# Performance work log

Hardware: AMD Instinct MI355X
Metric: run time of the kernel (lower is better)

The kernel has to match this reference:

```python
import jax, jax.numpy as jnp
import numpy as np

C = 32          # d_model / channels
D_STATE = 32
D_CONV = 4
EXPAND = 2
D_INNER = EXPAND * C          # 64
DT_RANK = (C + 15) // 16      # ceil(32/16) = 2
EPS = 1e-5


def _conv2d(x, w, b):
    # x: (B,C,H,W), w: (O,I,3,3), stride 1, padding 1 (torch Conv2d)
    y = jax.lax.conv_general_dilated(
        x, w, window_strides=(1, 1), padding=[(1, 1), (1, 1)],
        dimension_numbers=("NCHW", "OIHW", "NCHW"))
    return y + b[None, :, None, None]


def _silu(x):
    return x * jax.nn.sigmoid(x)


def _mamba(xs, in_proj_w, conv1d_w, conv1d_b, x_proj_w, dt_proj_w, dt_proj_b,
           A_log, Dp, out_proj_w):
    # xs: (B, L, C)
    xz = xs @ in_proj_w.T                       # (B, L, 2*D_INNER)
    xm, z = jnp.split(xz, 2, axis=-1)           # each (B, L, D_INNER)

    # causal depthwise conv1d along L (torch: padding=d_conv-1 then [..., :L])
    xc = xm.transpose(0, 2, 1)                  # (B, D_INNER, L)
    xc = jax.lax.conv_general_dilated(
        xc, conv1d_w, window_strides=(1,), padding=[(D_CONV - 1, 0)],
        dimension_numbers=("NCH", "OIH", "NCH"),
        feature_group_count=D_INNER)
    xm = _silu((xc + conv1d_b[None, :, None]).transpose(0, 2, 1))  # (B,L,D_INNER)

    x_dbl = xm @ x_proj_w.T                     # (B, L, DT_RANK + 2*D_STATE)
    dt = x_dbl[..., :DT_RANK]
    Bm = x_dbl[..., DT_RANK:DT_RANK + D_STATE]  # (B, L, N)
    Cm = x_dbl[..., DT_RANK + D_STATE:]         # (B, L, N)

    delta = jax.nn.softplus(dt @ dt_proj_w.T + dt_proj_b)  # (B, L, D_INNER)
    A = -jnp.exp(A_log)                                     # (D_INNER, N)

    deltaA = jnp.exp(delta[..., None] * A)                           # (B,L,D,N)
    deltaBx = delta[..., None] * Bm[:, :, None, :] * xm[..., None]   # (B,L,D,N)

    def combine(c1, c2):
        a1, b1 = c1
        a2, b2 = c2
        return a1 * a2, a2 * b1 + b2

    # parallel linear recurrence h_t = deltaA_t * h_{t-1} + deltaBx_t
    _, hstate = jax.lax.associative_scan(combine, (deltaA, deltaBx), axis=1)

    y = jnp.einsum("bldn,bln->bld", hstate, Cm) + xm * Dp
    y = y * _silu(z)
    return y @ out_proj_w.T                     # (B, L, C)


def setup_inputs() -> dict:
    key = jax.random.key(0)
    ks = jax.random.split(key, 16)
    s = 0.02
    inp = {
        "x": jax.random.normal(ks[0], (4, C, 64, 64), dtype=jnp.float32),
        "conv1_w": jax.random.normal(ks[1], (2 * C, C, 3, 3), jnp.float32) * s,
        "conv1_b": jnp.zeros((2 * C,), jnp.float32),
        "conv2_w": jax.random.normal(ks[2], (C, 2 * C, 3, 3), jnp.float32) * s,
        "conv2_b": jnp.zeros((C,), jnp.float32),
        "ln_g": jnp.ones((C,), jnp.float32),
        "ln_b": jnp.zeros((C,), jnp.float32),
        "in_proj_w": jax.random.normal(ks[3], (2 * D_INNER, C), jnp.float32) * s,
        "conv1d_w": jax.random.normal(ks[4], (D_INNER, 1, D_CONV), jnp.float32) * 0.1,
        "conv1d_b": jnp.zeros((D_INNER,), jnp.float32),
        "x_proj_w": jax.random.normal(ks[5], (DT_RANK + 2 * D_STATE, D_INNER), jnp.float32) * s,
        "dt_proj_w": jax.random.normal(ks[6], (D_INNER, DT_RANK), jnp.float32) * 0.1,
        "dt_proj_b": jax.random.normal(ks[7], (D_INNER,), jnp.float32) * 0.1 - 4.0,
        "A_log": jnp.log(jnp.tile(jnp.arange(1, D_STATE + 1, dtype=jnp.float32), (D_INNER, 1))),
        "Dp": jnp.ones((D_INNER,), jnp.float32),
        "out_proj_w": jax.random.normal(ks[8], (C, D_INNER), jnp.float32) * s,
        "smooth_w": jax.random.normal(ks[9], (C, C, 3, 3), jnp.float32) * s,
        "smooth_b": jnp.zeros((C,), jnp.float32),
    }
    return inp


def reference(x, conv1_w, conv1_b, conv2_w, conv2_b, ln_g, ln_b,
              in_proj_w, conv1d_w, conv1d_b, x_proj_w, dt_proj_w, dt_proj_b,
              A_log, Dp, out_proj_w, smooth_w, smooth_b):
    b, c, h, w = x.shape
    # convb residual
    t = jax.nn.relu(_conv2d(x, conv1_w, conv1_b))
    x = _conv2d(t, conv2_w, conv2_b) + x
    # reshape (b,c,h,w) -> (b, h*w, c) row-major (faithful to torch .reshape)
    xs = x.reshape(b, -1, c)
    # LayerNorm over last dim
    mu = jnp.mean(xs, axis=-1, keepdims=True)
    var = jnp.mean(jnp.square(xs - mu), axis=-1, keepdims=True)
    xs = (xs - mu) * jax.lax.rsqrt(var + EPS) * ln_g + ln_b
    # Mamba block
    y = _mamba(xs, in_proj_w, conv1d_w, conv1d_b, x_proj_w, dt_proj_w,
               dt_proj_b, A_log, Dp, out_proj_w)
    y = y.transpose(0, 2, 1).reshape(b, c, h, w)
    return _conv2d(y, smooth_w, smooth_b)
```

## Files before the change

### kernel.cpp

```cpp
#include <hip/hip_runtime.h>
#include <math.h>

#define SEQL 4096
#define L2E 1.44269504088896340736f

#if defined(__has_builtin)
#if __has_builtin(__builtin_amdgcn_exp2f)
#define FAST_EXP2(x) __builtin_amdgcn_exp2f(x)
#endif
#endif
#ifndef FAST_EXP2
#define FAST_EXP2(x) exp2f(x)
#endif

__device__ __forceinline__ float sigmoid_f(float x){ return 1.0f/(1.0f+expf(-x)); }

template<int CI, int CO, int COW, bool RELU, bool RES>
__global__ __launch_bounds__(512, 2) void conv3x3_k(const float* __restrict__ in,
    const float* __restrict__ wgt, const float* __restrict__ bias,
    const float* __restrict__ res, float* __restrict__ out)
{
  __shared__ __align__(16) float tin[CI][3][72];
  const int tid  = threadIdx.x;
  const int lane = tid & 63;
  const int ty   = tid >> 6;
  const int tyu  = __builtin_amdgcn_readfirstlane(ty);
  const int h0   = blockIdx.x;
  const int b    = blockIdx.y;
  const int co0  = tyu*COW;

  constexpr int NF4 = CI*48;
  #pragma unroll
  for (int k=0; k<NF4/512; ++k){
    int i   = tid + (k<<9);
    int ci  = i / 48;
    int rem = i - ci*48;
    int row = rem >> 4;
    int w4  = (rem & 15) << 2;
    int h   = h0 - 1 + row;
    float4 v = make_float4(0.f,0.f,0.f,0.f);
    if (h>=0 && h<64)
      v = *(const float4*)(in + ((size_t)(b*CI+ci)*64 + h)*64 + w4);
    *(float4*)&tin[ci][row][4+w4] = v;
    if (w4 == 0)  tin[ci][row][3]  = 0.0f;
    if (w4 == 60) tin[ci][row][68] = 0.0f;
  }
  __syncthreads();

  float acc[COW];
  #pragma unroll
  for (int u=0;u<COW;++u) acc[u] = 0.0f;

  #pragma unroll 2
  for (int ci=0; ci<CI; ++ci){
    float rv[3][3];
    #pragma unroll
    for (int r=0;r<3;++r)
      #pragma unroll
      for (int c=0;c<3;++c)
        rv[r][c] = tin[ci][r][3+lane+c];
    #pragma unroll
    for (int u=0;u<COW;++u){
      const float* wp = wgt + ((size_t)(co0+u)*CI + ci)*9;
      #pragma unroll
      for (int r=0;r<3;++r){
        acc[u] = fmaf(rv[r][0], wp[3*r+0], acc[u]);
        acc[u] = fmaf(rv[r][1], wp[3*r+1], acc[u]);
        acc[u] = fmaf(rv[r][2], wp[3*r+2], acc[u]);
      }
    }
  }

  #pragma unroll
  for (int u=0;u<COW;++u){
    float s = acc[u] + bias[co0+u];
    size_t ob = ((size_t)(b*CO+co0+u)*64 + h0)*64 + lane;
    if constexpr (RES)  s += res[ob];
    if constexpr (RELU) s = fmaxf(s, 0.0f);
    out[ob] = s;
  }
}

__global__ __launch_bounds__(1024, 4) void mamba_in_k(const float* __restrict__ x2,
    const float* __restrict__ g, const float* __restrict__ be,
    const float* __restrict__ Wip, const float* __restrict__ cw,
    const float* __restrict__ cb, const float* __restrict__ Wxp,
    const float* __restrict__ Wdt, const float* __restrict__ bdt,
    const float* __restrict__ A_log,
    float* __restrict__ xm2, float* __restrict__ szb, float* __restrict__ dlt,
    float* __restrict__ Bm, float* __restrict__ Cm,
    float* __restrict__ cA, float* __restrict__ cH)
{
  __shared__ __align__(16) float xn[68][37];
  __shared__ __align__(16) float xm[64][68];
  __shared__ __align__(16) float xtT[64][68];
  __shared__ __align__(16) float xd[64][67];
  float (*xbT)[68] = reinterpret_cast<float(*)[68]>(&xn[0][0]);
  const int tid = threadIdx.x, lane = tid & 63, ty = tid >> 6;
  const int tyu = __builtin_amdgcn_readfirstlane(ty);
  const int bi = blockIdx.x >> 6;
  const int l0 = (blockIdx.x & 63) << 6;

  {
    const int row = tid >> 3, sub = tid & 7;
    if (row < 67){
      const int tok = l0 - 3 + row;
      const int c0 = sub << 2;
      if (tok >= 0){
        float4 f = *(const float4*)(x2 + (size_t)bi*131072 + (size_t)tok*32 + c0);
        float s = (f.x+f.y)+(f.z+f.w);
        s += __shfl_xor(s,1); s += __shfl_xor(s,2); s += __shfl_xor(s,4);
        const float mu = s * 0.03125f;
        float dx=f.x-mu, dy=f.y-mu, dz=f.z-mu, dw=f.w-mu;
        float q = (dx*dx+dy*dy)+(dz*dz+dw*dw);
        q += __shfl_xor(q,1); q += __shfl_xor(q,2); q += __shfl_xor(q,4);
        const float rstd = 1.0f/sqrtf(q*0.03125f + 1e-5f);
        float4 gv = *(const float4*)(g  + c0);
        float4 bv = *(const float4*)(be + c0);
        xn[row][c0+0] = dx*rstd*gv.x + bv.x;
        xn[row][c0+1] = dy*rstd*gv.y + bv.y;
        xn[row][c0+2] = dz*rstd*gv.z + bv.z;
        xn[row][c0+3] = dw*rstd*gv.w + bv.w;
      } else {
        xn[row][c0+0]=0.0f; xn[row][c0+1]=0.0f;
        xn[row][c0+2]=0.0f; xn[row][c0+3]=0.0f;
      }
    }
  }
  __syncthreads();

  if (ty < 8){
    const int d0 = tyu*8;
    float xvA[32];
    #pragma unroll
    for (int c=0;c<32;++c) xvA[c] = xn[lane][c];
    #pragma unroll
    for (int jj=0;jj<8;++jj){
      const float4* wr = (const float4*)(Wip + (d0+jj)*32);
      float a = 0.0f;
      #pragma unroll
      for (int c4=0;c4<8;++c4){
        float4 w = wr[c4];
        a = fmaf(xvA[c4*4+0], w.x, a);
        a = fmaf(xvA[c4*4+1], w.y, a);
        a = fmaf(xvA[c4*4+2], w.z, a);
        a = fmaf(xvA[c4*4+3], w.w, a);
      }
      xm[d0+jj][lane] = a;
    }
    if (lane < 3){
      float xvB[32];
      #pragma unroll
      for (int c=0;c<32;++c) xvB[c] = xn[64+lane][c];
      #pragma unroll
      for (int jj=0;jj<8;++jj){
        const float4* wr = (const float4*)(Wip + (d0+jj)*32);
        float a = 0.0f;
        #pragma unroll
        for (int c4=0;c4<8;++c4){
          float4 w = wr[c4];
          a = fmaf(xvB[c4*4+0], w.x, a);
          a = fmaf(xvB[c4*4+1], w.y, a);
          a = fmaf(xvB[c4*4+2], w.z, a);
          a = fmaf(xvB[c4*4+3], w.w, a);
        }
        xm[d0+jj][64+lane] = a;
      }
    }
  } else {
    const int d0z = (tyu-8)*8;
    float xvC[32];
    #pragma unroll
    for (int c=0;c<32;++c) xvC[c] = xn[lane+3][c];
    #pragma unroll
    for (int jj=0;jj<8;++jj){
      const float4* wr = (const float4*)(Wip + (64+d0z+jj)*32);
      float a = 0.0f;
      #pragma unroll
      for (int c4=0;c4<8;++c4){
        float4 w = wr[c4];
        a = fmaf(xvC[c4*4+0], w.x, a);
        a = fmaf(xvC[c4*4+1], w.y, a);
        a = fmaf(xvC[c4*4+2], w.z, a);
        a = fmaf(xvC[c4*4+3], w.w, a);
      }
      szb[((size_t)(bi*64+d0z+jj))*SEQL + l0 + lane] = a * sigmoid_f(a);
    }
  }
  __syncthreads();

  #pragma unroll
  for (int jj=0;jj<4;++jj){
    int d = tyu*4 + jj;
    float4 w = *(const float4*)(cw + d*4);
    float a = xm[d][lane]*w.x + xm[d][lane+1]*w.y
            + xm[d][lane+2]*w.z + xm[d][lane+3]*w.w + cb[d];
    float s = a * sigmoid_f(a);
    xtT[d][lane] = s;
    xm2[((size_t)(bi*64+d))*SEQL + l0 + lane] = s;
  }
  __syncthreads();

  {
    float xv[64];
    #pragma unroll
    for (int c=0;c<64;++c) xv[c] = xtT[c][lane];
    for (int j=tyu; j<66; j+=16){
      const float4* wr = (const float4*)(Wxp + j*64);
      float a = 0.0f;
      #pragma unroll
      for (int c4=0;c4<16;++c4){
        float4 w = wr[c4];
        a = fmaf(xv[c4*4+0], w.x, a);
        a = fmaf(xv[c4*4+1], w.y, a);
        a = fmaf(xv[c4*4+2], w.z, a);
        a = fmaf(xv[c4*4+3], w.w, a);
      }
      xd[lane][j] = a;
    }
  }
  __syncthreads();

  {
    float dt0 = xd[lane][0], dt1 = xd[lane][1];
    #pragma unroll
    for (int k=0;k<4;++k){
      int d2 = tyu*4 + k;
      float2 wd = *(const float2*)(Wdt + d2*2);
      float v = dt0*wd.x + dt1*wd.y + bdt[d2];
      float sp = fmaxf(v,0.0f) + log1pf(expf(-fabsf(v)));
      dlt[((size_t)(bi*64+d2))*SEQL + l0 + lane] = sp;
      xm[d2][lane] = sp;
    }
    const int which = tyu >> 3, gq = tyu & 7;
    float* dst = which ? Cm : Bm;
    size_t base = ((size_t)bi*SEQL + l0 + lane)*32 + gq*4;
    const int s2 = 2 + which*32;
    float4 f0;
    f0.x = xd[lane][s2+gq+ 0]; f0.y = xd[lane][s2+gq+ 8];
    f0.z = xd[lane][s2+gq+16]; f0.w = xd[lane][s2+gq+24];
    *(float4*)(dst + base) = f0;
    if (!which){
      xbT[gq     ][lane] = f0.x;
      xbT[gq +  8][lane] = f0.y;
      xbT[gq + 16][lane] = f0.z;
      xbT[gq + 24][lane] = f0.w;
    }
  }
  __syncthreads();

  {
    const int d  = tid >> 4;
    const int gg = tid & 15;
    const int chunk = blockIdx.x & 63;
    const int bd = bi*64 + d;
    float Av0 = -expf(A_log[d*32 + gg     ]) * L2E;
    float Av1 = -expf(A_log[d*32 + gg + 16]) * L2E;
    float h0=0.0f, h1=0.0f, aP0=1.0f, aP1=1.0f;
    #pragma unroll 2
    for (int t0=0;t0<64;t0+=4){
      float4 dl4 = *(const float4*)&xm [d    ][t0];
      float4 xs4 = *(const float4*)&xtT[d    ][t0];
      float4 b04 = *(const float4*)&xbT[gg   ][t0];
      float4 b14 = *(const float4*)&xbT[gg+16][t0];
      #pragma unroll
      for (int k=0;k<4;++k){
        float dlv = (k==0)? dl4.x : (k==1)? dl4.y : (k==2)? dl4.z : dl4.w;
        float xsv = (k==0)? xs4.x : (k==1)? xs4.y : (k==2)? xs4.z : xs4.w;
        float bv0 = (k==0)? b04.x : (k==1)? b04.y : (k==2)? b04.z : b04.w;
        float bv1 = (k==0)? b14.x : (k==1)? b14.y : (k==2)? b14.z : b14.w;
        float m  = dlv * xsv;
        float a0 = FAST_EXP2(dlv*Av0);
        float a1 = FAST_EXP2(dlv*Av1);
        h0 = fmaf(a0, h0, m*bv0);  aP0 *= a0;
        h1 = fmaf(a1, h1, m*bv1);  aP1 *= a1;
      }
    }
    size_t base = ((size_t)bd*64 + chunk)*32;
    cA[base + gg] = aP0; cA[base + gg + 16] = aP1;
    cH[base + gg] = h0;  cH[base + gg + 16] = h1;
  }
}

__global__ __launch_bounds__(256) void scan_p2(const float* __restrict__ dlt,
    const float* __restrict__ xssm, const float* __restrict__ Bm,
    const float* __restrict__ Cm, const float* __restrict__ A_log,
    const float* __restrict__ Dp, const float* __restrict__ sz,
    const float* __restrict__ cA, const float* __restrict__ cHs,
    float* __restrict__ yt)
{
  __shared__ float pre[32][34];
  const int tid = threadIdx.x;
  const int grp = blockIdx.x & 1;
  const int bd  = blockIdx.x >> 1;
  const int b = bd >> 6, d = bd & 63;
  const int c0 = grp << 5;

  if (tid < 32){
    const float* pa = cA  + (size_t)bd*2048 + tid;
    const float* ph = cHs + (size_t)bd*2048 + tid;
    float hrun = 0.0f;
    if (grp){
      #pragma unroll 4
      for (int c=0;c<32;++c)
        hrun = fmaf(pa[c*32], hrun, ph[c*32]);
    }
    #pragma unroll 4
    for (int k=0;k<32;++k){
      pre[tid][k] = hrun;
      hrun = fmaf(pa[(c0+k)*32], hrun, ph[(c0+k)*32]);
    }
  }
  __syncthreads();

  const int lc = tid >> 3, gg = tid & 7;
  const int chunk = c0 + lc;
  const int l0 = chunk << 6;
  const float Dv = Dp[d];
  float Av2[4], h[4];
  #pragma unroll
  for (int j=0;j<4;++j){
    Av2[j] = -expf(A_log[d*32 + gg + 8*j]) * L2E;
    h[j] = pre[gg + 8*j][lc];
  }
  const float* del = dlt  + (size_t)bd*SEQL + l0;
  const float* xp  = xssm + (size_t)bd*SEQL + l0;
  const float* szp = sz   + (size_t)bd*SEQL + l0;
  const float* Bp  = Bm + ((size_t)b*SEQL + l0)*32 + gg*4;
  const float* Cp  = Cm + ((size_t)b*SEQL + l0)*32 + gg*4;
  float* yp = yt + (size_t)bd*SEQL + l0;

  for (int i0=0;i0<64;i0+=16){
    float4 y4[4];
    #pragma unroll
    for (int s=0;s<4;++s){
      const int ib = i0 + s*4;
      float4 d4 = *(const float4*)(del+ib);
      float4 x4 = *(const float4*)(xp +ib);
      float4 s4 = *(const float4*)(szp+ib);
      #pragma unroll
      for (int t=0;t<4;++t){
        float dl = (t==0)? d4.x : (t==1)? d4.y : (t==2)? d4.z : d4.w;
        float xl = (t==0)? x4.x : (t==1)? x4.y : (t==2)? x4.z : x4.w;
        float sl = (t==0)? s4.x : (t==1)? s4.y : (t==2)? s4.z : s4.w;
        float4 bv = *(const float4*)(Bp + (ib+t)*32);
        float4 cv = *(const float4*)(Cp + (ib+t)*32);
        float a0 = FAST_EXP2(dl*Av2[0]); h[0] = fmaf(a0, h[0], dl*bv.x*xl);
        float a1 = FAST_EXP2(dl*Av2[1]); h[1] = fmaf(a1, h[1], dl*bv.y*xl);
        float a2 = FAST_EXP2(dl*Av2[2]); h[2] = fmaf(a2, h[2], dl*bv.z*xl);
        float a3 = FAST_EXP2(dl*Av2[3]); h[3] = fmaf(a3, h[3], dl*bv.w*xl);
        float v = fmaf(h[3], cv.w, fmaf(h[2], cv.z, fmaf(h[1], cv.y, h[0]*cv.x)));
        v += __shfl_xor(v,1); v += __shfl_xor(v,2); v += __shfl_xor(v,4);
        float yv = fmaf(xl, Dv, v) * sl;
        if      (t==0) y4[s].x = yv;
        else if (t==1) y4[s].y = yv;
        else if (t==2) y4[s].z = yv;
        else           y4[s].w = yv;
      }
    }
    if (gg < 4){
      float4 w = (gg==0) ? y4[0] : (gg==1) ? y4[1] : (gg==2) ? y4[2] : y4[3];
      *(float4*)(yp + i0 + gg*4) = w;
    }
  }
}

__global__ __launch_bounds__(512) void outproj_k(const float* __restrict__ yt,
    const float* __restrict__ Wout, float* __restrict__ ym)
{
  __shared__ float ys[64][67];
  const int tid = threadIdx.x, lane = tid & 63, ty = tid >> 6;
  const int tyu = __builtin_amdgcn_readfirstlane(ty);
  const int bi = blockIdx.x >> 6;
  const int l0 = (blockIdx.x & 63) << 6;
  for (int r=ty; r<64; r+=8)
    ys[lane][r] = yt[((size_t)(bi*64+r))*SEQL + l0 + lane];
  __syncthreads();
  float yv[64];
  #pragma unroll
  for (int c=0;c<64;++c) yv[c] = ys[lane][c];
  #pragma unroll
  for (int jj=0;jj<4;++jj){
    int j = tyu*4 + jj;
    const float4* wr = (const float4*)(Wout + j*64);
    float acc = 0.0f;
    #pragma unroll
    for (int c4=0;c4<16;++c4){
      float4 w = wr[c4];
      acc = fmaf(yv[c4*4+0], w.x, acc);
      acc = fmaf(yv[c4*4+1], w.y, acc);
      acc = fmaf(yv[c4*4+2], w.z, acc);
      acc = fmaf(yv[c4*4+3], w.w, acc);
    }
    ym[((size_t)(bi*32+j))*SEQL + l0 + lane] = acc;
  }
}

extern "C" void kernel_launch(void* const* d_in, const int* in_sizes, int n_in,
                              void* d_out, int out_size, void* d_ws, size_t ws_size,
                              hipStream_t stream) {
  const float* x        = (const float*)d_in[0];
  const float* conv1_w  = (const float*)d_in[1];
  const float* conv1_b  = (const float*)d_in[2];
  const float* conv2_w  = (const float*)d_in[3];
  const float* conv2_b  = (const float*)d_in[4];
  const float* ln_g     = (const float*)d_in[5];
  const float* ln_b     = (const float*)d_in[6];
  const float* in_proj_w= (const float*)d_in[7];
  const float* conv1d_w = (const float*)d_in[8];
  const float* conv1d_b = (const float*)d_in[9];
  const float* x_proj_w = (const float*)d_in[10];
  const float* dt_proj_w= (const float*)d_in[11];
  const float* dt_proj_b= (const float*)d_in[12];
  const float* A_log    = (const float*)d_in[13];
  const float* Dp       = (const float*)d_in[14];
  const float* out_proj_w=(const float*)d_in[15];
  const float* smooth_w = (const float*)d_in[16];
  const float* smooth_b = (const float*)d_in[17];
  float* out = (float*)d_out;

  float* ws = (float*)d_ws;
  float* t      = ws;
  float* x2     = t      + 1048576;
  float* xm2    = x2     + 524288;
  float* szb    = xm2    + 1048576;
  float* dlt    = szb    + 1048576;
  float* Bmat   = dlt    + 1048576;
  float* Cmat   = Bmat   + 524288;
  float* yt     = Cmat   + 524288;
  float* ym     = yt     + 1048576;
  float* cA     = t;
  float* cH     = t + 524288;

  conv3x3_k<32,64,8,true ,false><<<dim3(64,4), 512, 0, stream>>>(x,  conv1_w, conv1_b, nullptr, t);
  conv3x3_k<64,32,4,false,true ><<<dim3(64,4), 512, 0, stream>>>(t,  conv2_w, conv2_b, x,       x2);
  mamba_in_k  <<<256, 1024, 0, stream>>>(x2, ln_g, ln_b, in_proj_w, conv1d_w, conv1d_b,
                                         x_proj_w, dt_proj_w, dt_proj_b, A_log,
                                         xm2, szb, dlt, Bmat, Cmat, cA, cH);
  scan_p2     <<<512, 256, 0, stream>>>(dlt, xm2, Bmat, Cmat, A_log, Dp, szb, cA, cH, yt);
  outproj_k   <<<256, 512, 0, stream>>>(yt, out_proj_w, ym);
  conv3x3_k<32,32,4,false,false><<<dim3(64,4), 512, 0, stream>>>(ym, smooth_w, smooth_b, nullptr, out);
}
```

Baseline: 219.4 us.

## Replace LDS-staged conv3x3 with direct global loads and wave shuffles

```diff
diff --git a/kernel.cpp b/kernel.cpp
--- a/kernel.cpp
+++ b/kernel.cpp
@@ -15,64 +15,48 @@
 
 __device__ __forceinline__ float sigmoid_f(float x){ return 1.0f/(1.0f+expf(-x)); }
 
-template<int CI, int CO, int COW, bool RELU, bool RES>
-__global__ __launch_bounds__(512, 2) void conv3x3_k(const float* __restrict__ in,
+template<int CI, int CO, int COG, bool RELU, bool RES>
+__global__ __launch_bounds__(256) void conv3x3_k(const float* __restrict__ in,
     const float* __restrict__ wgt, const float* __restrict__ bias,
     const float* __restrict__ res, float* __restrict__ out)
 {
-  __shared__ __align__(16) float tin[CI][3][72];
   const int tid  = threadIdx.x;
   const int lane = tid & 63;
   const int ty   = tid >> 6;
   const int tyu  = __builtin_amdgcn_readfirstlane(ty);
   const int h0   = blockIdx.x;
-  const int b    = blockIdx.y;
-  const int co0  = tyu*COW;
-
-  constexpr int NF4 = CI*48;
-  #pragma unroll
-  for (int k=0; k<NF4/512; ++k){
-    int i   = tid + (k<<9);
-    int ci  = i / 48;
-    int rem = i - ci*48;
-    int row = rem >> 4;
-    int w4  = (rem & 15) << 2;
-    int h   = h0 - 1 + row;
-    float4 v = make_float4(0.f,0.f,0.f,0.f);
-    if (h>=0 && h<64)
-      v = *(const float4*)(in + ((size_t)(b*CI+ci)*64 + h)*64 + w4);
-    *(float4*)&tin[ci][row][4+w4] = v;
-    if (w4 == 0)  tin[ci][row][3]  = 0.0f;
-    if (w4 == 60) tin[ci][row][68] = 0.0f;
-  }
-  __syncthreads();
-
-  float acc[COW];
-  #pragma unroll
-  for (int u=0;u<COW;++u) acc[u] = 0.0f;
+  const int co0  = (blockIdx.y*4 + tyu)*COG;
+  const int b    = blockIdx.z;
+
+  float acc[COG];
+  #pragma unroll
+  for (int u=0;u<COG;++u) acc[u] = 0.0f;
+
+  const float* inb = in + (size_t)b*CI*4096;
 
   #pragma unroll 2
   for (int ci=0; ci<CI; ++ci){
-    float rv[3][3];
-    #pragma unroll
-    for (int r=0;r<3;++r)
-      #pragma unroll
-      for (int c=0;c<3;++c)
-        rv[r][c] = tin[ci][r][3+lane+c];
-    #pragma unroll
-    for (int u=0;u<COW;++u){
-      const float* wp = wgt + ((size_t)(co0+u)*CI + ci)*9;
-      #pragma unroll
-      for (int r=0;r<3;++r){
-        acc[u] = fmaf(rv[r][0], wp[3*r+0], acc[u]);
-        acc[u] = fmaf(rv[r][1], wp[3*r+1], acc[u]);
-        acc[u] = fmaf(rv[r][2], wp[3*r+2], acc[u]);
-      }
-    }
-  }
-
-  #pragma unroll
-  for (int u=0;u<COW;++u){
+    const float* wb = wgt + ((size_t)co0*CI + ci)*9;
+    #pragma unroll
+    for (int r=0;r<3;++r){
+      const int h = h0 - 1 + r;
+      float v = 0.0f;
+      if (h>=0 && h<64)
+        v = inb[((size_t)ci*64 + h)*64 + lane];
+      float vl = __shfl_up(v, 1);
+      float vr = __shfl_down(v, 1);
+      if (lane == 0)  vl = 0.0f;
+      if (lane == 63) vr = 0.0f;
+      #pragma unroll
+      for (int u=0;u<COG;++u){
+        const float* wp = wb + (size_t)u*CI*9 + r*3;
+        acc[u] = fmaf(vl, wp[0], fmaf(v, wp[1], fmaf(vr, wp[2], acc[u])));
+      }
+    }
+  }
+
+  #pragma unroll
+  for (int u=0;u<COG;++u){
     float s = acc[u] + bias[co0+u];
     size_t ob = ((size_t)(b*CO+co0+u)*64 + h0)*64 + lane;
     if constexpr (RES)  s += res[ob];
@@ -432,12 +416,12 @@
   float* cA     = t;
   float* cH     = t + 524288;
 
-  conv3x3_k<32,64,8,true ,false><<<dim3(64,4), 512, 0, stream>>>(x,  conv1_w, conv1_b, nullptr, t);
-  conv3x3_k<64,32,4,false,true ><<<dim3(64,4), 512, 0, stream>>>(t,  conv2_w, conv2_b, x,       x2);
+  conv3x3_k<32,64,8,true ,false><<<dim3(64,2,4), 256, 0, stream>>>(x,  conv1_w, conv1_b, nullptr, t);
+  conv3x3_k<64,32,4,false,true ><<<dim3(64,2,4), 256, 0, stream>>>(t,  conv2_w, conv2_b, x,       x2);
   mamba_in_k  <<<256, 1024, 0, stream>>>(x2, ln_g, ln_b, in_proj_w, conv1d_w, conv1d_b,
                                          x_proj_w, dt_proj_w, dt_proj_b, A_log,
                                          xm2, szb, dlt, Bmat, Cmat, cA, cH);
   scan_p2     <<<512, 256, 0, stream>>>(dlt, xm2, Bmat, Cmat, A_log, Dp, szb, cA, cH, yt);
   outproj_k   <<<256, 512, 0, stream>>>(yt, out_proj_w, ym);
-  conv3x3_k<32,32,4,false,false><<<dim3(64,4), 512, 0, stream>>>(ym, smooth_w, smooth_b, nullptr, out);
+  conv3x3_k<32,32,4,false,false><<<dim3(64,2,4), 256, 0, stream>>>(ym, smooth_w, smooth_b, nullptr, out);
 }
```

After: 294.8 us. 1.34x slower.
